# Optimization experiments

Hardware: AMD Instinct MI355X
Metric: run time of the kernel (lower is better)

Reference implementation:

```python
import jax, jax.numpy as jnp
import numpy as np

N_FEAT = 512
N_HEAD = 8
CONTEXT_SIZES = (31, 61)
HEADS_PER_SCALE = N_HEAD // len(CONTEXT_SIZES)  # 4
B, T = 4, 2048


def _windows(v, cs):
    """Gather overlapping local windows (faithful to chunkwise with N_c=1).
    v: [B, T, D] -> [B, T, cs, D], zero-padded at both ends by (cs-1)//2."""
    Bv, Tv, D = v.shape
    half = (cs - 1) // 2
    vp = jnp.pad(v, ((0, 0), (half, half), (0, 0)))
    idx = jnp.arange(Tv)[:, None] + jnp.arange(cs)[None, :]  # [T, cs]
    return vp[:, idx, :]


def setup_inputs() -> dict:
    key0 = jax.random.key(0)
    ks = jax.random.split(key0, 12)
    s = 0.02
    inp = {
        "query": jax.random.normal(ks[0], (B, T, N_FEAT), jnp.float32),
        "key": jax.random.normal(ks[1], (B, T, N_FEAT), jnp.float32),
        "value": jax.random.normal(ks[2], (B, T, N_FEAT), jnp.float32),
        # Linear weights stored torch-style [out_features, in_features]
        "w1_0": jax.random.normal(ks[3], (N_FEAT, N_FEAT), jnp.float32) * s,
        "w1_1": jax.random.normal(ks[4], (N_FEAT, N_FEAT), jnp.float32) * s,
        "w2_0": jax.random.normal(ks[5], (HEADS_PER_SCALE * CONTEXT_SIZES[0], N_FEAT), jnp.float32) * s,
        "w2_1": jax.random.normal(ks[6], (HEADS_PER_SCALE * CONTEXT_SIZES[1], N_FEAT), jnp.float32) * s,
        "w3_0": jax.random.normal(ks[7], (N_FEAT, N_FEAT), jnp.float32) * s,
        "w3_1": jax.random.normal(ks[8], (N_FEAT, N_FEAT), jnp.float32) * s,
        "scale_weights": jnp.ones((len(CONTEXT_SIZES),), jnp.float32) / len(CONTEXT_SIZES),
        "w_out": jax.random.normal(ks[9], (N_FEAT, N_FEAT), jnp.float32) * s,
    }
    return inp


def reference(query, key, value, w1_0, w1_1, w2_0, w2_1, w3_0, w3_1, scale_weights, w_out):
    # key is unused by the original module's forward.
    Bq, Tq, Fq = query.shape
    hd = Fq // N_HEAD  # per-head dim within a scale after splitting n_feat by heads_per_scale? No:
    head_dim = Fq // HEADS_PER_SCALE  # matches original: D // heads_per_scale
    outs = []
    for (w1, w2, w3, cs) in ((w1_0, w2_0, w3_0, CONTEXT_SIZES[0]),
                             (w1_1, w2_1, w3_1, CONTEXT_SIZES[1])):
        q = query @ w1.T                      # [B,T,F]
        v = value @ w3.T                      # [B,T,F]
        logits = jax.nn.relu(q) @ w2.T        # [B,T,HS*cs]
        attn = jax.nn.softmax(logits.reshape(Bq, Tq, HEADS_PER_SCALE, cs), axis=-1)
        # local windows of v: [B,T,cs,F] -> [B,T,cs,HS,head_dim]
        vw = _windows(v, cs).reshape(Bq, Tq, cs, HEADS_PER_SCALE, head_dim)
        x = jnp.einsum('bthc,btchd->bthd', attn, vw).reshape(Bq, Tq, Fq)
        outs.append(x)
    sw = jax.nn.softmax(scale_weights)
    x = sw[0] * outs[0] + sw[1] * outs[1]
    return x @ w_out.T
```

## Files before the change

kernel.cpp:

```cpp
#include <hip/hip_runtime.h>

typedef unsigned short u16;
typedef unsigned long long u64;
typedef float floatx4 __attribute__((ext_vector_type(4)));
typedef short shortx8 __attribute__((ext_vector_type(8)));

__device__ inline u16 f2bf(float f) {
  unsigned u = __float_as_uint(f);
  u += 0x7fffu + ((u >> 16) & 1u);
  return (u16)(u >> 16);
}

__device__ __forceinline__ void gl16(const u16* g, const u16* l) {
  __builtin_amdgcn_global_load_lds(
      (const __attribute__((address_space(1))) unsigned int*)(u64)(const void*)g,
      (__attribute__((address_space(3))) unsigned int*)(unsigned)(u64)(const void*)l,
      16, 0, 0);
}

__global__ __launch_bounds__(256) void convert_all(
    const float* __restrict__ q, const float* __restrict__ v,
    const float* __restrict__ w10, const float* __restrict__ w11,
    const float* __restrict__ w30, const float* __restrict__ w31,
    const float* __restrict__ wo, const float* __restrict__ w20,
    const float* __restrict__ w21, u16* __restrict__ base) {
  size_t e = ((size_t)blockIdx.x * 256 + threadIdx.x) * 4;
  const float* src;
  u16* dst;
  size_t le;
  unsigned prows;
  if (e < 4194304ull)      { src = q;   dst = base;            le = e;            prows = 0x7fffffffu; }
  else if (e < 8388608ull) { src = v;   dst = base + 4194304;  le = e - 4194304;  prows = 0x7fffffffu; }
  else if (e < 8650752ull) { src = w10; dst = base + 8388608;  le = e - 8388608;  prows = 0x7fffffffu; }
  else if (e < 8912896ull) { src = w11; dst = base + 8650752;  le = e - 8650752;  prows = 0x7fffffffu; }
  else if (e < 9175040ull) { src = w30; dst = base + 8912896;  le = e - 8912896;  prows = 0x7fffffffu; }
  else if (e < 9437184ull) { src = w31; dst = base + 9175040;  le = e - 9175040;  prows = 0x7fffffffu; }
  else if (e < 9699328ull) { src = wo;  dst = base + 9437184;  le = e - 9437184;  prows = 0x7fffffffu; }
  else if (e < 9764864ull) { src = w20; dst = base + 9699328;  le = e - 9699328;  prows = 124; }
  else                     { src = w21; dst = base + 9764864;  le = e - 9764864;  prows = 244; }
  float4 val = make_float4(0.f, 0.f, 0.f, 0.f);
  if ((unsigned)(le >> 9) < prows) val = *(const float4*)(src + le);
  unsigned p0 = (unsigned)f2bf(val.x) | ((unsigned)f2bf(val.y) << 16);
  unsigned p1 = (unsigned)f2bf(val.z) | ((unsigned)f2bf(val.w) << 16);
  *(uint2*)(dst + le) = make_uint2(p0, p1);
}

template <int OUTBF>
__device__ __forceinline__ void gemm_core(
    const u16* __restrict__ A, int lda, const u16* __restrict__ W, int ldw,
    float* __restrict__ Cf, u16* __restrict__ Cb, int ldc, int relu,
    u16* lA, u16* lB) {
  const int tid = threadIdx.x;
  const int wave = tid >> 6, lane = tid & 63;
  const int wm = (wave >> 1) * 64, wn = (wave & 1) * 64;
  const int lr = lane & 15, kq = (lane >> 4) * 8;
  const int sr = lane >> 2, sc = (lane & 3) * 8;

  floatx4 acc[4][4];
#pragma unroll
  for (int i = 0; i < 4; ++i)
#pragma unroll
    for (int j = 0; j < 4; ++j) acc[i][j] = (floatx4){0.f, 0.f, 0.f, 0.f};

  const u16* ga0 = A + (u64)(wave * 32 + sr) * lda + sc;
  const u16* ga1 = A + (u64)(wave * 32 + 16 + sr) * lda + sc;
  const u16* gb0 = W + (u64)(wave * 32 + sr) * ldw + sc;
  const u16* gb1 = W + (u64)(wave * 32 + 16 + sr) * ldw + sc;
  u16* la0 = lA + (wave * 32) * 32;
  u16* la1 = lA + (wave * 32 + 16) * 32;
  u16* lb0 = lB + (wave * 32) * 32;
  u16* lb1 = lB + (wave * 32 + 16) * 32;

  for (int k0 = 0; k0 < 512; k0 += 32) {
    __syncthreads();
    gl16(ga0 + k0, la0);
    gl16(ga1 + k0, la1);
    gl16(gb0 + k0, lb0);
    gl16(gb1 + k0, lb1);
    __syncthreads();
    shortx8 af[4], bf8[4];
#pragma unroll
    for (int i = 0; i < 4; ++i) {
      af[i] = *(const shortx8*)&lA[(wm + i * 16 + lr) * 32 + kq];
      bf8[i] = *(const shortx8*)&lB[(wn + i * 16 + lr) * 32 + kq];
    }
#pragma unroll
    for (int mi = 0; mi < 4; ++mi)
#pragma unroll
      for (int ni = 0; ni < 4; ++ni)
        acc[mi][ni] = __builtin_amdgcn_mfma_f32_16x16x32_bf16(af[mi], bf8[ni], acc[mi][ni], 0, 0, 0);
  }
  const int er = wm + (lane >> 4) * 4;
  const int ec = wn + lr;
#pragma unroll
  for (int mi = 0; mi < 4; ++mi)
#pragma unroll
    for (int ni = 0; ni < 4; ++ni)
#pragma unroll
      for (int r = 0; r < 4; ++r) {
        float vv = acc[mi][ni][r];
        if (relu) vv = fmaxf(vv, 0.f);
        u64 off = (u64)(er + mi * 16 + r) * (u64)ldc + (u64)(ec + ni * 16);
        if (OUTBF) Cb[off] = f2bf(vv);
        else Cf[off] = vv;
      }
}

__global__ __launch_bounds__(256, 2) void k_qv(
    const u16* __restrict__ qb, const u16* __restrict__ vb,
    const u16* __restrict__ w1, const u16* __restrict__ w3,
    u16* __restrict__ rq, u16* __restrict__ vc) {
  __shared__ __align__(16) u16 lA[128 * 32];
  __shared__ __align__(16) u16 lB[128 * 32];
  const int bx = blockIdx.x, bn = blockIdx.y * 128;
  const bool isq = bx < 64;
  const int am = (isq ? bx : bx - 64) * 128;
  const u16* A = (isq ? qb : vb) + (u64)am * 512;
  const u16* W = (isq ? w1 : w3) + (u64)bn * 512;
  u16* Cb = (isq ? rq : vc) + (u64)am * 1024 + bn;
  gemm_core<1>(A, 512, W, 512, nullptr, Cb, 1024, isq ? 1 : 0, lA, lB);
}

__global__ __launch_bounds__(256, 2) void k_logits(
    const u16* __restrict__ rq, const u16* __restrict__ w20,
    const u16* __restrict__ w21, float* __restrict__ lg) {
  __shared__ __align__(16) u16 lA[128 * 32];
  __shared__ __align__(16) u16 lB[128 * 32];
  const int am = blockIdx.x * 128;
  const int y = blockIdx.y;
  const u16* A = rq + (u64)am * 1024 + (y == 0 ? 0 : 512);
  const u16* W = (y == 0) ? w20 : (w21 + (u64)(y - 1) * 128 * 512);
  float* Cf = lg + (u64)am * 384 + y * 128;
  gemm_core<0>(A, 1024, W, 512, Cf, nullptr, 384, 0, lA, lB);
}

__global__ __launch_bounds__(256, 2) void k_final(
    const u16* __restrict__ xb, const u16* __restrict__ wo,
    float* __restrict__ out) {
  __shared__ __align__(16) u16 lA[128 * 32];
  __shared__ __align__(16) u16 lB[128 * 32];
  const int am = blockIdx.x * 128, bn = blockIdx.y * 128;
  gemm_core<0>(xb + (u64)am * 512, 512, wo + (u64)bn * 512, 512,
               out + (u64)am * 512 + bn, nullptr, 512, 0, lA, lB);
}

#define VLDT 136
#define ESL 152

template <int CS, int CHUNK>
__device__ __forceinline__ void attn_mfma_pass(
    const float* __restrict__ lg,
    const u16* __restrict__ vbh,
    int bb, int t0, float swv,
    u16* vT, u16* es16, float* invsum, floatx4 (&o)[4]) {
  constexpr int HALF = (CS - 1) / 2;
  constexpr int NW = 64 + CS - 1;
  const int tid = threadIdx.x;
  const int wave = tid >> 6, lane = tid & 63;
  const int lr = lane & 15, kq = (lane >> 4) * 8;

  __syncthreads();

#pragma unroll
  for (int it = 0; it < 4; ++it) {
    int idx = it * 256 + tid;
    int r = idx >> 3;
    int dl8 = (idx & 7) * 8;
    int t = t0 + r - HALF;
    uint4 u = make_uint4(0u, 0u, 0u, 0u);
    if (r < NW && t >= 0 && t < 2048)
      u = *(const uint4*)&vbh[(u64)(bb + t) * 1024 + dl8];
    int sb = (((r >> 3) ^ ((dl8 >> 3) & 7)) << 3) + (r & 7);
    u16* wp = &vT[dl8 * VLDT + sb];
    const u16* us = (const u16*)&u;
#pragma unroll
    for (int j = 0; j < 8; ++j) wp[j * VLDT] = us[j];
  }

  {
    int tt = tid >> 2, qq = tid & 3;
    u16* row = es16 + tt * ESL;
    const int lo = tt, hi = tt + CS;
#pragma unroll
    for (int j = 0; j < 32; ++j) {
      int x = qq * 32 + j;
      if (x < lo || x >= hi) row[x] = 0;
    }
    const float* lrow = lg + (u64)(bb + t0 + tt) * 384 + qq * CHUNK;
    float ps = 0.f;
#pragma unroll
    for (int j = 0; j < CHUNK; ++j) {
      int c = qq * CHUNK + j;
      if (c < CS) {
        float ev = __expf(lrow[j]);
        row[lo + c] = f2bf(ev);
        ps += ev;
      }
    }
    ps += __shfl_xor(ps, 1, 64);
    ps += __shfl_xor(ps, 2, 64);
    if (qq == 0) invsum[tt] = swv / ps;
  }
  __syncthreads();

  const int kb_lo = (wave * 16) >> 5;
  const int kb_hi = (wave * 16 + 15 + CS - 1) >> 5;
  floatx4 acc[4];
#pragma unroll
  for (int nt = 0; nt < 4; ++nt) acc[nt] = (floatx4){0.f, 0.f, 0.f, 0.f};
  for (int kb = kb_lo; kb <= kb_hi; ++kb) {
    shortx8 af = *(const shortx8*)&es16[(wave * 16 + lr) * ESL + kb * 32 + kq];
    int rb8 = kb * 4 + (lane >> 4);
#pragma unroll
    for (int nt = 0; nt < 4; ++nt) {
      int d_row = nt * 16 + lr;
      int blk = (rb8 ^ ((d_row >> 3) & 7)) << 3;
      shortx8 bf8 = *(const shortx8*)&vT[d_row * VLDT + blk];
      acc[nt] = __builtin_amdgcn_mfma_f32_16x16x32_bf16(af, bf8, acc[nt], 0, 0, 0);
    }
  }
  float invs[4];
#pragma unroll
  for (int rr = 0; rr < 4; ++rr)
    invs[rr] = invsum[wave * 16 + (lane >> 4) * 4 + rr];
#pragma unroll
  for (int nt = 0; nt < 4; ++nt)
#pragma unroll
    for (int rr = 0; rr < 4; ++rr) o[nt][rr] += acc[nt][rr] * invs[rr];
}

__global__ __launch_bounds__(256, 2) void k_attn4(
    const float* __restrict__ lg, const u16* __restrict__ vcat,
    const float* __restrict__ swp, u16* __restrict__ xbw) {
  __shared__ __align__(16) u16 vT[64 * VLDT];
  __shared__ __align__(16) u16 es16[64 * ESL];
  __shared__ float invsum[64];
  const int tid = threadIdx.x;
  const int wave = tid >> 6, lane = tid & 63;
  const int lr = lane & 15;
  const int t0 = blockIdx.x * 64;
  const int h = blockIdx.y >> 1, dh = blockIdx.y & 1;
  const int b = blockIdx.z;
  const int bb = b * 2048;
  const int m0 = bb + t0;

  float a0 = swp[0], a1 = swp[1];
  float mx = fmaxf(a0, a1);
  float e0 = __expf(a0 - mx), e1 = __expf(a1 - mx);
  float inv = 1.f / (e0 + e1);

  floatx4 o[4];
#pragma unroll
  for (int nt = 0; nt < 4; ++nt) o[nt] = (floatx4){0.f, 0.f, 0.f, 0.f};

  attn_mfma_pass<31, 8>(lg + h * 31, vcat + h * 128 + dh * 64,
                        bb, t0, e0 * inv, vT, es16, invsum, o);
  attn_mfma_pass<61, 16>(lg + 128 + h * 61, vcat + 512 + h * 128 + dh * 64,
                         bb, t0, e1 * inv, vT, es16, invsum, o);

  __syncthreads();
#pragma unroll
  for (int nt = 0; nt < 4; ++nt)
#pragma unroll
    for (int rr = 0; rr < 4; ++rr) {
      int trow = wave * 16 + (lane >> 4) * 4 + rr;
      es16[trow * ESL + nt * 16 + lr] = f2bf(o[nt][rr]);
    }
  __syncthreads();
#pragma unroll
  for (int rep = 0; rep < 2; ++rep) {
    int idx = rep * 256 + tid;
    int trow = idx >> 3;
    int col8 = (idx & 7) * 8;
    uint4 u = *(const uint4*)&es16[trow * ESL + col8];
    *(uint4*)&xbw[(u64)(m0 + trow) * 512 + h * 128 + dh * 64 + col8] = u;
  }
}

extern "C" void kernel_launch(void* const* d_in, const int* in_sizes, int n_in,
                              void* d_out, int out_size, void* d_ws, size_t ws_size,
                              hipStream_t stream) {
  const float* q   = (const float*)d_in[0];
  const float* v   = (const float*)d_in[2];
  const float* w10 = (const float*)d_in[3];
  const float* w11 = (const float*)d_in[4];
  const float* w20 = (const float*)d_in[5];
  const float* w21 = (const float*)d_in[6];
  const float* w30 = (const float*)d_in[7];
  const float* w31 = (const float*)d_in[8];
  const float* sw  = (const float*)d_in[9];
  const float* wo  = (const float*)d_in[10];
  float* out = (float*)d_out;

  u16* base  = (u16*)d_ws;
  u16* qb    = base;
  u16* vb    = base + 4194304;
  u16* w1cat = base + 8388608;
  u16* w3cat = base + 8912896;
  u16* wob   = base + 9437184;
  u16* w2b0  = base + 9699328;
  u16* w2b1  = base + 9764864;
  char* fb = (char*)d_ws + 19791872;
  float* logitsC = (float*)fb;
  u16* rqcat = (u16*)(logitsC + 3145728);
  u16* vcat  = rqcat + 8388608;
  u16* xb    = vcat + 8388608;

  convert_all<<<dim3(9664), dim3(256), 0, stream>>>(q, v, w10, w11, w30, w31, wo, w20, w21, base);

  dim3 blk(256);
  k_qv<<<dim3(128, 8), blk, 0, stream>>>(qb, vb, w1cat, w3cat, rqcat, vcat);
  k_logits<<<dim3(64, 3), blk, 0, stream>>>(rqcat, w2b0, w2b1, logitsC);
  k_attn4<<<dim3(32, 8, 4), blk, 0, stream>>>(logitsC, vcat, sw, xb);
  k_final<<<dim3(64, 4), blk, 0, stream>>>(xb, wob, out);
}
```

Baseline: 172.1 us.

## Replace q/v projection GEMM with 256x256-tile, 8-wave pipelined kernel

The q/v projection GEMM moves from 128x128 tiles with 256 threads to a hand-scheduled 256x256 tile kernel with 512 threads and 128KB dynamic LDS. It double-buffers global-to-LDS loads with explicit vmcnt waits, uses XOR-swizzled LDS layouts, raises MFMA priority with setprio, and remaps block ids to group tiles. The goal is more operand reuse per LDS load and better overlap of memory with MFMA. In exchange it needs much more LDS and registers, which limits occupancy.

New measurement: 169.8 us. Within noise of the previous version (-1.3%).

```diff
diff --git a/kernel.cpp b/kernel.cpp
--- a/kernel.cpp
+++ b/kernel.cpp
@@ -106,19 +106,169 @@
       }
 }
 
-__global__ __launch_bounds__(256, 2) void k_qv(
+__global__ __launch_bounds__(512, 2) void k_qv8(
     const u16* __restrict__ qb, const u16* __restrict__ vb,
     const u16* __restrict__ w1, const u16* __restrict__ w3,
     u16* __restrict__ rq, u16* __restrict__ vc) {
-  __shared__ __align__(16) u16 lA[128 * 32];
-  __shared__ __align__(16) u16 lB[128 * 32];
-  const int bx = blockIdx.x, bn = blockIdx.y * 128;
-  const bool isq = bx < 64;
-  const int am = (isq ? bx : bx - 64) * 128;
-  const u16* A = (isq ? qb : vb) + (u64)am * 512;
-  const u16* W = (isq ? w1 : w3) + (u64)bn * 512;
-  u16* Cb = (isq ? rq : vc) + (u64)am * 1024 + bn;
-  gemm_core<1>(A, 512, W, 512, nullptr, Cb, 1024, isq ? 1 : 0, lA, lB);
+  extern __shared__ __align__(16) u16 lds[];
+  const int bid = blockIdx.x;
+  const int bx = (bid & 7) * 32 + (bid >> 3);
+  const bool isq = bx < 128;
+  const int lb = isq ? bx : bx - 128;
+  const int m0 = (lb >> 2) * 256;
+  const int n0 = (lb & 3) * 256;
+  const u16* __restrict__ A = isq ? qb : vb;
+  const u16* __restrict__ W = isq ? w1 : w3;
+  u16* __restrict__ C = isq ? rq : vc;
+
+  const int tid = threadIdx.x;
+  const int wv = tid >> 6, lane = tid & 63;
+  const int wr = wv >> 2, wc = wv & 3;
+  const int lr = lane & 15, kq = lane >> 4;
+
+  const unsigned Ca = ((unsigned)((lr >> 1) & 7)) << 3;
+  const unsigned afb = ((unsigned)((wr * 128 + lr) * 32 + kq * 8)) ^ Ca;
+  const unsigned bfb = ((unsigned)((wc * 32 + lr) * 32 + kq * 8)) ^ Ca;
+
+  const unsigned u0 = (unsigned)(wv * 1024 + lane * 8);
+  const unsigned u1 = u0 + 512;
+  const unsigned g0 = u0 ^ (((u0 >> 6) & 7) << 3);
+  const unsigned g1 = u1 ^ (((u1 >> 6) & 7) << 3);
+  const unsigned gA0 = (unsigned)(m0 + (int)(g0 >> 5)) * 512u + (g0 & 31);
+  const unsigned gA1 = (unsigned)(m0 + (int)(g1 >> 5)) * 512u + (g1 & 31);
+  const unsigned rp0 = (g0 >> 5) & 127, rp1 = (g1 >> 5) & 127;
+  const unsigned gB0n0 = (unsigned)(n0 + (int)((rp0 >> 5) * 64 + (rp0 & 31))) * 512u
+                         + (g0 >> 12) * 32 + (g0 & 31);
+  const unsigned gB1n0 = (unsigned)(n0 + (int)((rp1 >> 5) * 64 + (rp1 & 31))) * 512u
+                         + (g1 >> 12) * 32 + (g1 & 31);
+  const unsigned gB0n1 = gB0n0 + 32u * 512u;
+  const unsigned gB1n1 = gB1n0 + 32u * 512u;
+  const unsigned wvo = (unsigned)wv * 1024u;
+
+#define SA(d, kk, ga, gb, ko) \
+  gl16(A + (ga) + (ko), lds + (d)*16384 + (kk)*8192 + wvo); \
+  gl16(A + (gb) + (ko), lds + (d)*16384 + (kk)*8192 + wvo + 512)
+#define SB(d, nh, ga, gb, ko) \
+  gl16(W + (ga) + (ko), lds + 32768 + (d)*16384 + (nh)*8192 + wvo); \
+  gl16(W + (gb) + (ko), lds + 32768 + (d)*16384 + (nh)*8192 + wvo + 512)
+#define LOAD_AF(kk, d) \
+  _Pragma("unroll") \
+  for (int m = 0; m < 8; ++m) \
+    af[m] = *(const shortx8*)&lds[(d)*16384 + (kk)*8192 + afb + (unsigned)m * 512]
+#define LOAD_BF(kk, nh, d) \
+  bf0 = *(const shortx8*)&lds[32768 + (d)*16384 + (nh)*8192 + (kk)*4096 + bfb]; \
+  bf1 = *(const shortx8*)&lds[32768 + (d)*16384 + (nh)*8192 + (kk)*4096 + bfb + 512]
+#define MFMA16(nh) \
+  __builtin_amdgcn_s_setprio(1); \
+  _Pragma("unroll") \
+  for (int m = 0; m < 8; ++m) { \
+    acc[m][(nh)*2]   = __builtin_amdgcn_mfma_f32_16x16x32_bf16(af[m], bf0, acc[m][(nh)*2], 0, 0, 0); \
+    acc[m][(nh)*2+1] = __builtin_amdgcn_mfma_f32_16x16x32_bf16(af[m], bf1, acc[m][(nh)*2+1], 0, 0, 0); \
+  } \
+  __builtin_amdgcn_s_setprio(0)
+#define BAR() \
+  __builtin_amdgcn_sched_barrier(0); \
+  __builtin_amdgcn_s_barrier(); \
+  asm volatile("" ::: "memory"); \
+  __builtin_amdgcn_sched_barrier(0)
+#define WAITVM4() \
+  __builtin_amdgcn_sched_barrier(0); \
+  asm volatile("s_waitcnt vmcnt(4)" ::: "memory"); \
+  __builtin_amdgcn_sched_barrier(0)
+#define WAITVM0() \
+  __builtin_amdgcn_sched_barrier(0); \
+  asm volatile("s_waitcnt vmcnt(0)" ::: "memory"); \
+  __builtin_amdgcn_sched_barrier(0)
+
+  floatx4 acc[8][4];
+#pragma unroll
+  for (int m = 0; m < 8; ++m)
+#pragma unroll
+    for (int n = 0; n < 4; ++n) acc[m][n] = (floatx4){0.f, 0.f, 0.f, 0.f};
+  shortx8 af[8], bf0, bf1;
+
+  SA(0, 0, gA0, gA1, 0);
+  SB(0, 0, gB0n0, gB1n0, 0);
+  SA(0, 1, gA0 + 32, gA1 + 32, 0);
+  SB(0, 1, gB0n1, gB1n1, 0);
+  SA(1, 0, gA0, gA1, 64);
+  SB(1, 0, gB0n0, gB1n0, 64);
+  WAITVM4();
+  BAR();
+
+#pragma unroll 1
+  for (int i = 0; i < 3; ++i) {
+    const unsigned k1 = (unsigned)(2 * i + 1) * 64u;
+    const unsigned k2 = k1 + 64u, k3 = k1 + 128u;
+    SA(1, 1, gA0 + 32, gA1 + 32, k1);
+    LOAD_AF(0, 0); LOAD_BF(0, 0, 0); MFMA16(0);
+    BAR();
+    SB(1, 1, gB0n1, gB1n1, k1);
+    LOAD_BF(0, 1, 0); MFMA16(1);
+    BAR();
+    SA(0, 0, gA0, gA1, k2);
+    LOAD_AF(1, 0); LOAD_BF(1, 0, 0); MFMA16(0);
+    BAR();
+    SB(0, 0, gB0n0, gB1n0, k2);
+    LOAD_BF(1, 1, 0); MFMA16(1);
+    WAITVM4();
+    BAR();
+    SA(0, 1, gA0 + 32, gA1 + 32, k2);
+    LOAD_AF(0, 1); LOAD_BF(0, 0, 1); MFMA16(0);
+    BAR();
+    SB(0, 1, gB0n1, gB1n1, k2);
+    LOAD_BF(0, 1, 1); MFMA16(1);
+    BAR();
+    SA(1, 0, gA0, gA1, k3);
+    LOAD_AF(1, 1); LOAD_BF(1, 0, 1); MFMA16(0);
+    BAR();
+    SB(1, 0, gB0n0, gB1n0, k3);
+    LOAD_BF(1, 1, 1); MFMA16(1);
+    WAITVM4();
+    BAR();
+  }
+  {
+    const unsigned k1 = 448u;
+    SA(1, 1, gA0 + 32, gA1 + 32, k1);
+    LOAD_AF(0, 0); LOAD_BF(0, 0, 0); MFMA16(0);
+    BAR();
+    SB(1, 1, gB0n1, gB1n1, k1);
+    LOAD_BF(0, 1, 0); MFMA16(1);
+    BAR();
+    LOAD_AF(1, 0); LOAD_BF(1, 0, 0); MFMA16(0);
+    BAR();
+    LOAD_BF(1, 1, 0); MFMA16(1);
+    WAITVM0();
+    BAR();
+    LOAD_AF(0, 1); LOAD_BF(0, 0, 1); MFMA16(0);
+    BAR();
+    LOAD_BF(0, 1, 1); MFMA16(1);
+    BAR();
+    LOAD_AF(1, 1); LOAD_BF(1, 0, 1); MFMA16(0);
+    BAR();
+    LOAD_BF(1, 1, 1); MFMA16(1);
+  }
+
+  const int er0 = m0 + wr * 128 + (lane >> 4) * 4;
+  const int ec0 = n0 + wc * 64 + lr;
+#pragma unroll
+  for (int m = 0; m < 8; ++m)
+#pragma unroll
+    for (int n = 0; n < 4; ++n)
+#pragma unroll
+      for (int r = 0; r < 4; ++r) {
+        float vv = acc[m][n][r];
+        if (isq) vv = fmaxf(vv, 0.f);
+        C[(u64)(er0 + m * 16 + r) * 1024 + (u64)(ec0 + n * 16)] = f2bf(vv);
+      }
+#undef SA
+#undef SB
+#undef LOAD_AF
+#undef LOAD_BF
+#undef MFMA16
+#undef BAR
+#undef WAITVM4
+#undef WAITVM0
 }
 
 __global__ __launch_bounds__(256, 2) void k_logits(
@@ -306,10 +456,17 @@
   u16* vcat  = rqcat + 8388608;
   u16* xb    = vcat + 8388608;
 
+  static bool attr_done = false;
+  if (!attr_done) {
+    hipFuncSetAttribute((const void*)k_qv8,
+                        hipFuncAttributeMaxDynamicSharedMemorySize, 131072);
+    attr_done = true;
+  }
+
   convert_all<<<dim3(9664), dim3(256), 0, stream>>>(q, v, w10, w11, w30, w31, wo, w20, w21, base);
 
   dim3 blk(256);
-  k_qv<<<dim3(128, 8), blk, 0, stream>>>(qb, vb, w1cat, w3cat, rqcat, vcat);
+  k_qv8<<<dim3(256), dim3(512), 131072, stream>>>(qb, vb, w1cat, w3cat, rqcat, vcat);
   k_logits<<<dim3(64, 3), blk, 0, stream>>>(rqcat, w2b0, w2b1, logitsC);
   k_attn4<<<dim3(32, 8, 4), blk, 0, stream>>>(logitsC, vcat, sw, xb);
   k_final<<<dim3(64, 4), blk, 0, stream>>>(xb, wob, out);
```

## Widen QV projection GEMM to 128x256 tiles with 512-thread blocks and swizzled order

Applied to the files above, without the earlier changes.

Replaces the shared 128x128 GEMM core for the Q/V projections with a dedicated kernel that uses 512 threads (8 waves) computing 128x256 output tiles. Each A tile is reused across twice as many output columns, and a block-index swizzle spreads neighbouring tiles across XCDs. It adds register and LDS pressure (launch bounds ask for 4 blocks per CU) and keeps a single-buffered loop with two barriers per K step.

New measurement: 173.4 us. About the same (+0.8%).

```diff
diff --git a/kernel.cpp b/kernel.cpp
--- a/kernel.cpp
+++ b/kernel.cpp
@@ -106,19 +106,73 @@
       }
 }
 
-__global__ __launch_bounds__(256, 2) void k_qv(
+__global__ __launch_bounds__(512, 4) void k_qv9(
     const u16* __restrict__ qb, const u16* __restrict__ vb,
     const u16* __restrict__ w1, const u16* __restrict__ w3,
     u16* __restrict__ rq, u16* __restrict__ vc) {
   __shared__ __align__(16) u16 lA[128 * 32];
-  __shared__ __align__(16) u16 lB[128 * 32];
-  const int bx = blockIdx.x, bn = blockIdx.y * 128;
-  const bool isq = bx < 64;
-  const int am = (isq ? bx : bx - 64) * 128;
-  const u16* A = (isq ? qb : vb) + (u64)am * 512;
-  const u16* W = (isq ? w1 : w3) + (u64)bn * 512;
-  u16* Cb = (isq ? rq : vc) + (u64)am * 1024 + bn;
-  gemm_core<1>(A, 512, W, 512, nullptr, Cb, 1024, isq ? 1 : 0, lA, lB);
+  __shared__ __align__(16) u16 lB[256 * 32];
+  const int bid = blockIdx.x;
+  const int lb = (bid & 7) * 64 + (bid >> 3);
+  const bool isq = lb < 256;
+  const int lq = lb & 255;
+  const int m0 = (lq >> 2) * 128;
+  const int n0 = (lq & 3) * 256;
+  const u16* __restrict__ A = isq ? qb : vb;
+  const u16* __restrict__ W = isq ? w1 : w3;
+  u16* __restrict__ C = isq ? rq : vc;
+
+  const int tid = threadIdx.x;
+  const int wv = tid >> 6, lane = tid & 63;
+  const int wm = (wv >> 2) * 64;
+  const int wn = (wv & 3) * 64;
+  const int lr = lane & 15, kq = (lane >> 4) * 8;
+  const int sr = lane >> 2, sc = (lane & 3) * 8;
+
+  floatx4 acc[4][4];
+#pragma unroll
+  for (int i = 0; i < 4; ++i)
+#pragma unroll
+    for (int j = 0; j < 4; ++j) acc[i][j] = (floatx4){0.f, 0.f, 0.f, 0.f};
+
+  const u16* ga0 = A + (u64)(m0 + wv * 16 + sr) * 512 + sc;
+  const u16* gb0 = W + (u64)(n0 + wv * 32 + sr) * 512 + sc;
+  const u16* gb1 = W + (u64)(n0 + wv * 32 + 16 + sr) * 512 + sc;
+  u16* la0 = lA + (wv * 16) * 32;
+  u16* lb0 = lB + (wv * 32) * 32;
+  u16* lb1 = lB + (wv * 32 + 16) * 32;
+
+  for (int k0 = 0; k0 < 512; k0 += 32) {
+    __syncthreads();
+    gl16(ga0 + k0, la0);
+    gl16(gb0 + k0, lb0);
+    gl16(gb1 + k0, lb1);
+    __syncthreads();
+    shortx8 af[4], bf8[4];
+#pragma unroll
+    for (int i = 0; i < 4; ++i) {
+      af[i] = *(const shortx8*)&lA[(wm + i * 16 + lr) * 32 + kq];
+      bf8[i] = *(const shortx8*)&lB[(wn + i * 16 + lr) * 32 + kq];
+    }
+#pragma unroll
+    for (int mi = 0; mi < 4; ++mi)
+#pragma unroll
+      for (int ni = 0; ni < 4; ++ni)
+        acc[mi][ni] = __builtin_amdgcn_mfma_f32_16x16x32_bf16(af[mi], bf8[ni], acc[mi][ni], 0, 0, 0);
+  }
+
+  const int er = m0 + wm + (lane >> 4) * 4;
+  const int ec = n0 + wn + lr;
+#pragma unroll
+  for (int mi = 0; mi < 4; ++mi)
+#pragma unroll
+    for (int ni = 0; ni < 4; ++ni)
+#pragma unroll
+      for (int r = 0; r < 4; ++r) {
+        float vv = acc[mi][ni][r];
+        if (isq) vv = fmaxf(vv, 0.f);
+        C[(u64)(er + mi * 16 + r) * 1024 + (u64)(ec + ni * 16)] = f2bf(vv);
+      }
 }
 
 __global__ __launch_bounds__(256, 2) void k_logits(
@@ -309,7 +363,7 @@
   convert_all<<<dim3(9664), dim3(256), 0, stream>>>(q, v, w10, w11, w30, w31, wo, w20, w21, base);
 
   dim3 blk(256);
-  k_qv<<<dim3(128, 8), blk, 0, stream>>>(qb, vb, w1cat, w3cat, rqcat, vcat);
+  k_qv9<<<dim3(512), dim3(512), 0, stream>>>(qb, vb, w1cat, w3cat, rqcat, vcat);
   k_logits<<<dim3(64, 3), blk, 0, stream>>>(rqcat, w2b0, w2b1, logitsC);
   k_attn4<<<dim3(32, 8, 4), blk, 0, stream>>>(logitsC, vcat, sw, xb);
   k_final<<<dim3(64, 4), blk, 0, stream>>>(xb, wob, out);
```
